# Optimization experiments

Hardware: AMD Instinct MI355X
Metric: run time of the kernel (lower is better)

The kernel has to match this reference:

```python
import jax, jax.numpy as jnp
import numpy as np

N = 100000   # nodes
E = 800000   # directed edges (before self-loops)
D = 64       # hidden_dim
NUM_ROUNDS = 4
EPS = 1e-5


def setup_inputs() -> dict:
    key = jax.random.key(0)
    k0, k1, k2 = jax.random.split(key, 3)
    x = jax.random.normal(k0, (N, D), dtype=jnp.float32)
    edge_index = jax.random.randint(k1, (2, E), 0, N, dtype=jnp.int32)
    W = jax.random.normal(k2, (D, D), dtype=jnp.float32) * (1.0 / np.sqrt(D))
    b = jnp.zeros((D,), dtype=jnp.float32)
    gamma = jnp.ones((D,), dtype=jnp.float32)
    beta = jnp.zeros((D,), dtype=jnp.float32)
    return {"x": x, "edge_index": edge_index, "W": W, "b": b,
            "gamma": gamma, "beta": beta, "num_rounds": NUM_ROUNDS}


def reference(x, edge_index, W, b, gamma, beta, num_rounds):
    n = x.shape[0]
    # GCNConv: add self-loops, symmetric degree normalization D^-1/2 (A+I) D^-1/2
    loops = jnp.arange(n, dtype=edge_index.dtype)
    src = jnp.concatenate([edge_index[0], loops])  # [E+N] message sources
    dst = jnp.concatenate([edge_index[1], loops])  # [E+N] message targets
    deg = jax.ops.segment_sum(jnp.ones_like(dst, dtype=x.dtype), dst, num_segments=n)
    dis = jnp.where(deg > 0, jax.lax.rsqrt(deg), 0.0)  # deg^-1/2, 0 for isolated
    norm = dis[src] * dis[dst]                          # [E+N] edge weights

    for _ in range(num_rounds):
        h = x @ W                                                      # [N, D]
        msgs = h[src] * norm[:, None]                                  # gather [E+N, D]
        agg = jax.ops.segment_sum(msgs, dst, num_segments=n) + b      # scatter-add
        # LayerNorm over feature dim
        mu = agg.mean(axis=-1, keepdims=True)
        var = agg.var(axis=-1, keepdims=True)
        x = (agg - mu) * jax.lax.rsqrt(var + EPS) * gamma + beta
    return x
```

## Files before the change

kernel.cpp:

```cpp
#include <hip/hip_runtime.h>

#define D 64
#define EPSV 1e-5f
#define SLOTP 16
#define SLOTS2 24

typedef _Float16 f16;
typedef _Float16 f16x8 __attribute__((ext_vector_type(8)));
typedef float f32x4 __attribute__((ext_vector_type(4)));


__global__ void k_init(int* cursor, int n) {
    int i = blockIdx.x * blockDim.x + threadIdx.x;
    if (i < n) cursor[i] = 0;
}

__global__ void k_fill(const int* __restrict__ src, const int* __restrict__ dst,
                       int* __restrict__ cursor, unsigned* __restrict__ slots,
                       unsigned* __restrict__ slots2, int e) {
    const int t = blockIdx.x * blockDim.x + threadIdx.x;
    const int stride = gridDim.x * blockDim.x;
    int sv[4], dv[4]; bool ok[4];
#pragma unroll
    for (int k = 0; k < 4; ++k) {
        int i = t + k * stride;
        ok[k] = (i < e);
        int ii = ok[k] ? i : 0;
        sv[k] = src[ii]; dv[k] = dst[ii];
    }
#pragma unroll
    for (int k = 0; k < 4; ++k) {
        if (!ok[k]) continue;
        int d_ = dv[k];
        int p = atomicAdd(&cursor[d_], 1);
        if (p < SLOTP) {
            slots[(size_t)d_ * SLOTP + p] = (unsigned)sv[k];
        } else if (p < SLOTP + SLOTS2) {
            slots2[(size_t)d_ * SLOTS2 + (p - SLOTP)] = (unsigned)sv[k];
        }
    }
}

__global__ void k_dis(const int* __restrict__ cursor, float* __restrict__ disv, int n) {
    int i = blockIdx.x * blockDim.x + threadIdx.x;
    if (i < n) disv[i] = rsqrtf((float)(cursor[i] + 1));
}

__global__ void k_wpack(const float* __restrict__ W, f16* __restrict__ Wp) {
    int idx = blockIdx.x * blockDim.x + threadIdx.x;
    if (idx >= 512) return;
    int s = idx >> 8, rem = idx & 255, t = rem >> 6, l = rem & 63;
    int q = l >> 4, c = l & 15;
#pragma unroll
    for (int j = 0; j < 8; ++j) {
        int k = 32 * s + 8 * q + j;
        Wp[(size_t)idx * 8 + j] = (f16)W[k * D + 16 * t + c];
    }
}

__global__ __launch_bounds__(256) void k_xform(
    const float* __restrict__ x, const f16* __restrict__ Wp,
    const float* __restrict__ disv, f16* __restrict__ h, int n, int ntiles) {
    const int wv = blockIdx.x * 4 + (threadIdx.x >> 6);
    const int lane = threadIdx.x & 63;
    const int q = lane >> 4, c = lane & 15;

    const f16x8* wp = (const f16x8*)Wp;
    f16x8 w0 = wp[0 * 64 + lane], w1 = wp[1 * 64 + lane];
    f16x8 w2 = wp[2 * 64 + lane], w3 = wp[3 * 64 + lane];
    f16x8 w4 = wp[4 * 64 + lane], w5 = wp[5 * 64 + lane];
    f16x8 w6 = wp[6 * 64 + lane], w7 = wp[7 * 64 + lane];

#pragma unroll
    for (int tt = 0; tt < 2; ++tt) {
        const int tile = wv * 2 + tt;
        if (tile >= ntiles) break;
        const int row0 = tile * 16;
        const int rA = (row0 + c < n) ? (row0 + c) : (n - 1);

        const float4* xr = (const float4*)(x + (size_t)rA * D);
        float4 u0 = xr[2 * q], u1 = xr[2 * q + 1];
        float4 u2 = xr[8 + 2 * q], u3 = xr[9 + 2 * q];
        f16x8 a0 = (f16x8){(f16)u0.x, (f16)u0.y, (f16)u0.z, (f16)u0.w,
                           (f16)u1.x, (f16)u1.y, (f16)u1.z, (f16)u1.w};
        f16x8 a1 = (f16x8){(f16)u2.x, (f16)u2.y, (f16)u2.z, (f16)u2.w,
                           (f16)u3.x, (f16)u3.y, (f16)u3.z, (f16)u3.w};

        f32x4 d0 = {0,0,0,0}, d1 = {0,0,0,0}, d2 = {0,0,0,0}, d3 = {0,0,0,0};
        d0 = __builtin_amdgcn_mfma_f32_16x16x32_f16(a0, w0, d0, 0, 0, 0);
        d1 = __builtin_amdgcn_mfma_f32_16x16x32_f16(a0, w1, d1, 0, 0, 0);
        d2 = __builtin_amdgcn_mfma_f32_16x16x32_f16(a0, w2, d2, 0, 0, 0);
        d3 = __builtin_amdgcn_mfma_f32_16x16x32_f16(a0, w3, d3, 0, 0, 0);
        d0 = __builtin_amdgcn_mfma_f32_16x16x32_f16(a1, w4, d0, 0, 0, 0);
        d1 = __builtin_amdgcn_mfma_f32_16x16x32_f16(a1, w5, d1, 0, 0, 0);
        d2 = __builtin_amdgcn_mfma_f32_16x16x32_f16(a1, w6, d2, 0, 0, 0);
        d3 = __builtin_amdgcn_mfma_f32_16x16x32_f16(a1, w7, d3, 0, 0, 0);

        f32x4 dvv = *(const f32x4*)(disv + row0 + 4 * q);
#pragma unroll
        for (int r = 0; r < 4; ++r) {
            int row = row0 + q * 4 + r;
            if (row < n) {
                f16* hr = h + (size_t)row * D + c;
                hr[0]  = (f16)(d0[r] * dvv[r]);
                hr[16] = (f16)(d1[r] * dvv[r]);
                hr[32] = (f16)(d2[r] * dvv[r]);
                hr[48] = (f16)(d3[r] * dvv[r]);
            }
        }
    }
}

template<bool LAST>
__global__ __launch_bounds__(256) void k_fuse(
    const f16* __restrict__ h, const unsigned* __restrict__ slots,
    const unsigned* __restrict__ slots2, const int* __restrict__ cursor,
    const float* __restrict__ disv,
    const float* __restrict__ bb, const float* __restrict__ gamma,
    const float* __restrict__ beta, const f16* __restrict__ Wp,
    float* __restrict__ out, f16* __restrict__ hnext, int n) {
    __shared__ __align__(16) f16 ylds[32][72];

    const int tid = threadIdx.x;
    const int grp = tid >> 3;
    const int fl  = tid & 7;
    const int w = blockIdx.x * 32 + grp;
    const bool act = (w < n);

    if (act) {
        const int jb = w * SLOTP;
        const int dg = cursor[w];
        const int dgp = (dg < SLOTP) ? dg : SLOTP;

        float acc[8];
        {
            f16x8 sv = *(const f16x8*)(h + (size_t)w * D + fl * 8);
#pragma unroll
            for (int f = 0; f < 8; ++f) acc[f] = (float)sv[f];
        }

        uint4 s0 = *(const uint4*)(slots + jb);
        uint4 s1 = *(const uint4*)(slots + jb + 4);
        uint4 s2 = *(const uint4*)(slots + jb + 8);
        const unsigned idx[12] = {s0.x, s0.y, s0.z, s0.w,
                                  s1.x, s1.y, s1.z, s1.w,
                                  s2.x, s2.y, s2.z, s2.w};
        f16x8 v[12];
#pragma unroll
        for (int k = 0; k < 12; ++k) {
            unsigned u = (k < dg) ? idx[k] : 0u;
            v[k] = *(const f16x8*)(h + (size_t)u * D + fl * 8);
        }
#pragma unroll
        for (int k = 0; k < 12; ++k) {
            float m = (k < dg) ? 1.0f : 0.0f;
#pragma unroll
            for (int f = 0; f < 8; ++f) acc[f] += m * (float)v[k][f];
        }
        if (dgp > 12) {
            uint4 sr = *(const uint4*)(slots + jb + 12);
            const unsigned uu[4] = {sr.x, sr.y, sr.z, sr.w};
#pragma unroll
            for (int k = 0; k < 4; ++k) {
                unsigned u = (12 + k < dgp) ? uu[k] : 0u;
                float m = (12 + k < dgp) ? 1.0f : 0.0f;
                f16x8 vv = *(const f16x8*)(h + (size_t)u * D + fl * 8);
#pragma unroll
                for (int f = 0; f < 8; ++f) acc[f] += m * (float)vv[f];
            }
        }
        if (dg > SLOTP) {
            const unsigned* r2 = slots2 + (size_t)w * SLOTS2;
            int dg2 = dg - SLOTP; if (dg2 > SLOTS2) dg2 = SLOTS2;
#pragma unroll
            for (int base = 0; base < SLOTS2; base += 4) {
                if (base < dg2) {
                    uint4 sr = *(const uint4*)(r2 + base);
                    const unsigned uu[4] = {sr.x, sr.y, sr.z, sr.w};
#pragma unroll
                    for (int k = 0; k < 4; ++k) {
                        unsigned u = (base + k < dg2) ? uu[k] : 0u;
                        float m = (base + k < dg2) ? 1.0f : 0.0f;
                        f16x8 vv = *(const f16x8*)(h + (size_t)u * D + fl * 8);
#pragma unroll
                        for (int f = 0; f < 8; ++f) acc[f] += m * (float)vv[f];
                    }
                }
            }
        }

        const float dv = disv[w];
        const float4 b0 = ((const float4*)bb)[fl * 2],    b1 = ((const float4*)bb)[fl * 2 + 1];
        const float4 g0 = ((const float4*)gamma)[fl * 2], g1 = ((const float4*)gamma)[fl * 2 + 1];
        const float4 e0 = ((const float4*)beta)[fl * 2],  e1 = ((const float4*)beta)[fl * 2 + 1];
        const float bs[8] = {b0.x, b0.y, b0.z, b0.w, b1.x, b1.y, b1.z, b1.w};
        const float gs[8] = {g0.x, g0.y, g0.z, g0.w, g1.x, g1.y, g1.z, g1.w};
        const float es[8] = {e0.x, e0.y, e0.z, e0.w, e1.x, e1.y, e1.z, e1.w};

#pragma unroll
        for (int f = 0; f < 8; ++f) acc[f] = acc[f] * dv + bs[f];

        float s = 0.0f;
#pragma unroll
        for (int f = 0; f < 8; ++f) s += acc[f];
#pragma unroll
        for (int m = 1; m < 8; m <<= 1) s += __shfl_xor(s, m);
        float mu = s * (1.0f / 64.0f);
        float dd[8], qv = 0.0f;
#pragma unroll
        for (int f = 0; f < 8; ++f) { dd[f] = acc[f] - mu; qv += dd[f] * dd[f]; }
#pragma unroll
        for (int m = 1; m < 8; m <<= 1) qv += __shfl_xor(qv, m);
        float rstd = rsqrtf(qv * (1.0f / 64.0f) + EPSV);

        if (LAST) {
            float4 o0, o1;
            o0.x = dd[0] * rstd * gs[0] + es[0]; o0.y = dd[1] * rstd * gs[1] + es[1];
            o0.z = dd[2] * rstd * gs[2] + es[2]; o0.w = dd[3] * rstd * gs[3] + es[3];
            o1.x = dd[4] * rstd * gs[4] + es[4]; o1.y = dd[5] * rstd * gs[5] + es[5];
            o1.z = dd[6] * rstd * gs[6] + es[6]; o1.w = dd[7] * rstd * gs[7] + es[7];
            float4* orow = (float4*)(out + (size_t)w * D);
            orow[fl * 2] = o0; orow[fl * 2 + 1] = o1;
        } else {
            f16x8 yv;
#pragma unroll
            for (int f = 0; f < 8; ++f) yv[f] = (f16)(dd[f] * rstd * gs[f] + es[f]);
            *(f16x8*)(&ylds[grp][fl * 8]) = yv;
        }
    }
    if (LAST) return;

    __syncthreads();

    const int wv = tid >> 6;
    const int lane = tid & 63;
    const int q = lane >> 4, c = lane & 15;

    const f16x8* wp = (const f16x8*)Wp;
    f16x8 wlo = wp[wv * 64 + lane];
    f16x8 whi = wp[(4 + wv) * 64 + lane];

    const int row0 = blockIdx.x * 32;
#pragma unroll
    for (int rt = 0; rt < 2; ++rt) {
        f16x8 a0 = *(const f16x8*)(&ylds[rt * 16 + c][q * 8]);
        f16x8 a1 = *(const f16x8*)(&ylds[rt * 16 + c][32 + q * 8]);
        f32x4 d = {0, 0, 0, 0};
        d = __builtin_amdgcn_mfma_f32_16x16x32_f16(a0, wlo, d, 0, 0, 0);
        d = __builtin_amdgcn_mfma_f32_16x16x32_f16(a1, whi, d, 0, 0, 0);

        const int rbase = row0 + rt * 16;
        f32x4 dvv = *(const f32x4*)(disv + rbase + 4 * q);
#pragma unroll
        for (int r = 0; r < 4; ++r) {
            int row = rbase + q * 4 + r;
            if (row < n)
                hnext[(size_t)row * D + wv * 16 + c] = (f16)(d[r] * dvv[r]);
        }
    }
}


extern "C" void kernel_launch(void* const* d_in, const int* in_sizes, int n_in,
                              void* d_out, int out_size, void* d_ws, size_t ws_size,
                              hipStream_t stream) {
    const float* x0    = (const float*)d_in[0];
    const int*   ei    = (const int*)d_in[1];
    const float* W     = (const float*)d_in[2];
    const float* b     = (const float*)d_in[3];
    const float* gamma = (const float*)d_in[4];
    const float* beta  = (const float*)d_in[5];

    const int N = in_sizes[0] / D;
    const int E = in_sizes[1] / 2;
    const int* src = ei;
    const int* dst = ei + E;

    char* ws = (char*)d_ws;
    size_t off = 0;
    auto alloc = [&](size_t bytes) {
        off = (off + 255) & ~(size_t)255;
        void* p = ws + off;
        off += bytes;
        return p;
    };
    int*      cursor = (int*)alloc((size_t)N * 4);
    unsigned* slots  = (unsigned*)alloc((size_t)N * SLOTP * 4);
    unsigned* slots2 = (unsigned*)alloc((size_t)N * SLOTS2 * 4);
    float*    disv   = (float*)alloc((size_t)(N + 32) * 4);
    f16*      Wp     = (f16*)alloc(512 * 8 * 2);
    f16*      hA     = (f16*)alloc((size_t)N * D * 2);
    f16*      hB     = (f16*)alloc((size_t)N * D * 2);
    (void)ws_size;

    const int nbN = (N + 255) / 256;
    const int nbF = (E + 1023) / 1024;

    k_init<<<nbN, 256, 0, stream>>>(cursor, N);
    k_fill<<<nbF, 256, 0, stream>>>(src, dst, cursor, slots, slots2, E);
    k_dis <<<nbN, 256, 0, stream>>>(cursor, disv, N);
    k_wpack<<<2, 256, 0, stream>>>(W, Wp);

    float* out = (float*)d_out;
    const int ntiles = (N + 15) / 16;
    const int nwav   = (ntiles + 1) / 2;
    const int GX = (nwav + 3) / 4;
    const int GG = (N + 31) / 32;

    k_xform<<<GX, 256, 0, stream>>>(x0, Wp, disv, hA, N, ntiles);
    k_fuse<false><<<GG, 256, 0, stream>>>(hA, slots, slots2, cursor, disv, b, gamma,
                                          beta, Wp, nullptr, hB, N);
    k_fuse<false><<<GG, 256, 0, stream>>>(hB, slots, slots2, cursor, disv, b, gamma,
                                          beta, Wp, nullptr, hA, N);
    k_fuse<false><<<GG, 256, 0, stream>>>(hA, slots, slots2, cursor, disv, b, gamma,
                                          beta, Wp, nullptr, hB, N);
    k_fuse<true><<<GG, 256, 0, stream>>>(hB, slots, slots2, cursor, disv, b, gamma,
                                         beta, Wp, out, nullptr, N);
}
```

Baseline: 241.9 us.

## Build adjacency slots via two-pass bucketed binning instead of global atomics

Replaces the per-edge global atomic fill of destination slot lists with a two-phase binning: first edges are partitioned into 512-node buckets with shared-memory counting and a per-block global reservation, then each bucket is processed by one block that assigns slots using shared-memory atomics and writes slot rows with coalesced vector stores. The aim is to remove scattered global atomics and random global writes during graph preprocessing. It adds an intermediate bucket buffer with fixed capacity (8192 per bucket) and packs source ids into 17 bits, which assumes N fits in 2^17 and that buckets do not overflow. Slot order within a node may also change, which alters floating-point summation order.

```diff
diff --git a/kernel.cpp b/kernel.cpp
--- a/kernel.cpp
+++ b/kernel.cpp
@@ -4,41 +4,88 @@
 #define EPSV 1e-5f
 #define SLOTP 16
 #define SLOTS2 24
+#define BSH 9
+#define BNODES (1 << BSH)
+#define BCAP 8192
+#define SRCBITS 17
 
 typedef _Float16 f16;
 typedef _Float16 f16x8 __attribute__((ext_vector_type(8)));
 typedef float f32x4 __attribute__((ext_vector_type(4)));
 
 
-__global__ void k_init(int* cursor, int n) {
+__global__ void k_init(int* gcnt, int nbk) {
     int i = blockIdx.x * blockDim.x + threadIdx.x;
-    if (i < n) cursor[i] = 0;
-}
-
-__global__ void k_fill(const int* __restrict__ src, const int* __restrict__ dst,
-                       int* __restrict__ cursor, unsigned* __restrict__ slots,
-                       unsigned* __restrict__ slots2, int e) {
-    const int t = blockIdx.x * blockDim.x + threadIdx.x;
-    const int stride = gridDim.x * blockDim.x;
-    int sv[4], dv[4]; bool ok[4];
-#pragma unroll
-    for (int k = 0; k < 4; ++k) {
-        int i = t + k * stride;
-        ok[k] = (i < e);
-        int ii = ok[k] ? i : 0;
-        sv[k] = src[ii]; dv[k] = dst[ii];
-    }
-#pragma unroll
-    for (int k = 0; k < 4; ++k) {
-        if (!ok[k]) continue;
-        int d_ = dv[k];
-        int p = atomicAdd(&cursor[d_], 1);
-        if (p < SLOTP) {
-            slots[(size_t)d_ * SLOTP + p] = (unsigned)sv[k];
-        } else if (p < SLOTP + SLOTS2) {
-            slots2[(size_t)d_ * SLOTS2 + (p - SLOTP)] = (unsigned)sv[k];
-        }
-    }
+    if (i < nbk) gcnt[i] = 0;
+}
+
+__global__ __launch_bounds__(256) void k_binA(
+    const int* __restrict__ src, const int* __restrict__ dst,
+    int* __restrict__ gcnt, unsigned* __restrict__ breg, int e, int nbk) {
+    __shared__ int bcnt[256];
+    __shared__ int gbase[256];
+    const int tid = threadIdx.x;
+    if (tid < nbk) bcnt[tid] = 0;
+    __syncthreads();
+
+    const int per = (e + gridDim.x - 1) / gridDim.x;
+    const int lo = blockIdx.x * per;
+    const int hi = min(e, lo + per);
+
+    for (int i = lo + tid; i < hi; i += 256)
+        atomicAdd(&bcnt[dst[i] >> BSH], 1);
+    __syncthreads();
+
+    if (tid < nbk) {
+        int c = bcnt[tid];
+        gbase[tid] = (c > 0) ? atomicAdd(&gcnt[tid], c) : 0;
+        bcnt[tid] = 0;
+    }
+    __syncthreads();
+
+    for (int i = lo + tid; i < hi; i += 256) {
+        int d_ = dst[i], s_ = src[i];
+        int bkt = d_ >> BSH;
+        int p = gbase[bkt] + atomicAdd(&bcnt[bkt], 1);
+        if (p < BCAP)
+            breg[(size_t)bkt * BCAP + p] =
+                ((unsigned)(d_ & (BNODES - 1)) << SRCBITS) | (unsigned)s_;
+    }
+}
+
+__global__ __launch_bounds__(256) void k_binB(
+    const int* __restrict__ gcnt, const unsigned* __restrict__ breg,
+    unsigned* __restrict__ slots, unsigned* __restrict__ slots2,
+    int* __restrict__ cursor, int n) {
+    __shared__ int scnt[BNODES];
+    __shared__ unsigned sbuf[BNODES][SLOTP];
+    const int tid = threadIdx.x;
+    const int bkt = blockIdx.x;
+    const int base = bkt << BSH;
+    const int nloc = min(BNODES, n - base);
+
+    for (int i = tid; i < BNODES; i += 256) scnt[i] = 0;
+    __syncthreads();
+
+    const int cnt = min(gcnt[bkt], BCAP);
+    const unsigned* reg = breg + (size_t)bkt * BCAP;
+    for (int i = tid; i < cnt; i += 256) {
+        unsigned v = reg[i];
+        int ld = v >> SRCBITS;
+        unsigned s = v & ((1u << SRCBITS) - 1);
+        int p = atomicAdd(&scnt[ld], 1);
+        if (p < SLOTP) sbuf[ld][p] = s;
+        else if (p < SLOTP + SLOTS2)
+            slots2[(size_t)(base + ld) * SLOTS2 + (p - SLOTP)] = s;
+    }
+    __syncthreads();
+
+    for (int i = tid; i < nloc * 4; i += 256) {
+        int ld = i >> 2, part = i & 3;
+        ((uint4*)(slots + (size_t)(base + ld) * SLOTP))[part] =
+            ((const uint4*)sbuf[ld])[part];
+    }
+    for (int i = tid; i < nloc; i += 256) cursor[base + i] = scnt[i];
 }
 
 __global__ void k_dis(const int* __restrict__ cursor, float* __restrict__ disv, int n) {
@@ -275,6 +322,7 @@
     const int E = in_sizes[1] / 2;
     const int* src = ei;
     const int* dst = ei + E;
+    const int nbk = (N + BNODES - 1) >> BSH;
 
     char* ws = (char*)d_ws;
     size_t off = 0;
@@ -287,6 +335,8 @@
     int*      cursor = (int*)alloc((size_t)N * 4);
     unsigned* slots  = (unsigned*)alloc((size_t)N * SLOTP * 4);
     unsigned* slots2 = (unsigned*)alloc((size_t)N * SLOTS2 * 4);
+    int*      gcnt   = (int*)alloc((size_t)nbk * 4);
+    unsigned* breg   = (unsigned*)alloc((size_t)nbk * BCAP * 4);
     float*    disv   = (float*)alloc((size_t)(N + 32) * 4);
     f16*      Wp     = (f16*)alloc(512 * 8 * 2);
     f16*      hA     = (f16*)alloc((size_t)N * D * 2);
@@ -294,10 +344,10 @@
     (void)ws_size;
 
     const int nbN = (N + 255) / 256;
-    const int nbF = (E + 1023) / 1024;
-
-    k_init<<<nbN, 256, 0, stream>>>(cursor, N);
-    k_fill<<<nbF, 256, 0, stream>>>(src, dst, cursor, slots, slots2, E);
+
+    k_init<<<1, 256, 0, stream>>>(gcnt, nbk);
+    k_binA<<<128, 256, 0, stream>>>(src, dst, gcnt, breg, E, nbk);
+    k_binB<<<nbk, 256, 0, stream>>>(gcnt, breg, slots, slots2, cursor, N);
     k_dis <<<nbN, 256, 0, stream>>>(cursor, disv, N);
     k_wpack<<<2, 256, 0, stream>>>(W, Wp);
 
```

New measurement: 219.8 us. -9.2%, faster.
